# Performance work log

Hardware: AMD Instinct MI355X
Metric: run time of the kernel (lower is better)

Reference implementation:

```python
import jax, jax.numpy as jnp
import numpy as np

B, S, F, D, H, L = 32, 512, 10, 768, 12, 12
DK = D // H
FF = 4 * D
EPS = 1e-6
NEG = -1e9


def make_pe(window, d):
    pos = np.arange(window)[:, None].astype(np.float64)
    pe = np.zeros((window, d))
    ie = np.arange(0, d, 2)
    pe[:, 0::2] = np.sin(pos / 10000 ** (2 * ie / d))
    io = np.arange(1, d, 2)
    pe[:, 1::2] = np.cos(pos / 10000 ** (2 * (io + 1) / d))
    return jnp.asarray(pe, jnp.float32)


def setup_inputs() -> dict:
    key = jax.random.key(0)
    ks = jax.random.split(key, 20)
    s = 0.02
    inp = {
        "x": jax.random.normal(ks[0], (B, S, F), jnp.float32),
        "mask": jax.random.randint(ks[1], (B, S), 0, 2, jnp.int32),
        "w_emb": jax.random.normal(ks[2], (F, D), jnp.float32) * s,
        "b_emb": jnp.zeros((D,), jnp.float32),
        "pe": make_pe(S, D),
        "wq": jax.random.normal(ks[3], (L, D, D), jnp.float32) * s,
        "bq": jnp.zeros((L, D), jnp.float32),
        "wk": jax.random.normal(ks[4], (L, D, D), jnp.float32) * s,
        "bk": jnp.zeros((L, D), jnp.float32),
        "wv": jax.random.normal(ks[5], (L, D, D), jnp.float32) * s,
        "bv": jnp.zeros((L, D), jnp.float32),
        "wo": jax.random.normal(ks[6], (L, D, D), jnp.float32) * s,
        "bo": jnp.zeros((L, D), jnp.float32),
        "w1": jax.random.normal(ks[7], (L, D, FF), jnp.float32) * s,
        "b1": jnp.zeros((L, FF), jnp.float32),
        "w2": jax.random.normal(ks[8], (L, FF, D), jnp.float32) * s,
        "b2": jnp.zeros((L, D), jnp.float32),
        "ln1_a": jnp.ones((L, D), jnp.float32),
        "ln1_b": jnp.zeros((L, D), jnp.float32),
        "ln2_a": jnp.ones((L, D), jnp.float32),
        "ln2_b": jnp.zeros((L, D), jnp.float32),
    }
    return inp


def _ln(x, a, b):
    # torch-style: unbiased std (ddof=1) and divide by (std + eps)
    m = jnp.mean(x, -1, keepdims=True)
    var = jnp.sum((x - m) ** 2, -1, keepdims=True) / (x.shape[-1] - 1)
    return a * (x - m) / (jnp.sqrt(var) + EPS) + b


def _gelu(x):
    c = np.sqrt(2.0 / np.pi).astype(np.float32)
    return 0.5 * x * (1.0 + jnp.tanh(c * (x + 0.044715 * x ** 3)))


def _block(h, p, mask_b):
    wq, bq, wk, bk, wv, bv, wo, bo, w1, b1, w2, b2, a1, c1, a2, c2 = p
    y = _ln(h, a1, c1)
    q = (jnp.einsum('bsd,de->bse', y, wq) + bq).reshape(B, S, H, DK).transpose(0, 2, 1, 3)
    k = (jnp.einsum('bsd,de->bse', y, wk) + bk).reshape(B, S, H, DK).transpose(0, 2, 1, 3)
    v = (jnp.einsum('bsd,de->bse', y, wv) + bv).reshape(B, S, H, DK).transpose(0, 2, 1, 3)
    scores = jnp.einsum('bhqd,bhkd->bhqk', q, k) / np.sqrt(DK).astype(np.float32)
    scores = jnp.where(mask_b, scores, NEG)
    p_attn = jax.nn.softmax(scores, axis=-1)
    o = jnp.einsum('bhqk,bhkd->bhqd', p_attn, v).transpose(0, 2, 1, 3).reshape(B, S, D)
    h = h + (jnp.einsum('bsd,de->bse', o, wo) + bo)
    y2 = _ln(h, a2, c2)
    ff = jnp.einsum('bsf,fd->bsd', _gelu(jnp.einsum('bsd,df->bsf', y2, w1) + b1), w2) + b2
    return h + ff


def reference(x, mask, w_emb, b_emb, pe, wq, bq, wk, bk, wv, bv, wo, bo,
              w1, b1, w2, b2, ln1_a, ln1_b, ln2_a, ln2_b):
    # mask -> [B,1,1,S] boolean, broadcast over query positions (== repeat in torch)
    mask_b = (mask > 0)[:, None, None, :]
    h = jnp.einsum('bsf,fd->bsd', x, w_emb) + b_emb                 # InputEmbedding
    h = h * jnp.sqrt(jnp.float32(D)) + pe[None, :S]                 # PositionalEncoding
    params = (wq, bq, wk, bk, wv, bv, wo, bo, w1, b1, w2, b2,
              ln1_a, ln1_b, ln2_a, ln2_b)
    h, _ = jax.lax.scan(lambda c, p: (_block(c, p, mask_b), None), h, params)
    return h
```

## Files before the change

kernel.cpp:

```cpp
#include <hip/hip_runtime.h>
#include <cstdint>
#include <cstddef>

typedef unsigned short u16;
typedef __attribute__((ext_vector_type(8))) short s16x8;
typedef __attribute__((ext_vector_type(4))) float f32x4;

#define N_B 32
#define N_S 512
#define N_F 10
#define N_D 768
#define N_H 12
#define N_L 12
#define N_FF 3072
#define TOK (N_B*N_S)

__device__ __forceinline__ u16 f2bf(float f){
  union { float f; unsigned u; } x; x.f = f;
  unsigned r = x.u + 0x7fffu + ((x.u >> 16) & 1u);
  return (u16)(r >> 16);
}

__device__ __forceinline__ void gload16(const void* g, void* l){
  typedef const __attribute__((address_space(1))) unsigned GU;
  typedef __attribute__((address_space(3))) unsigned LU;
  __builtin_amdgcn_global_load_lds((GU*)(uintptr_t)g, (LU*)(uintptr_t)l, 16, 0, 0);
}

__global__ __launch_bounds__(256) void conv_t(const float* __restrict__ src,
                                              u16* __restrict__ dst, int K, int N)
{
  __shared__ float t[32][33];
  const size_t moff = (size_t)blockIdx.z * K * N;
  const float* s = src + moff;
  u16* d = dst + moff;
  const int k0 = blockIdx.x*32, n0 = blockIdx.y*32;
  const int tx = threadIdx.x, ty = threadIdx.y;
  #pragma unroll
  for (int i = 0; i < 32; i += 8)
    t[ty+i][tx] = s[(size_t)(k0+ty+i)*N + n0 + tx];
  __syncthreads();
  #pragma unroll
  for (int i = 0; i < 32; i += 8)
    d[(size_t)(n0+ty+i)*K + k0 + tx] = f2bf(t[tx][ty+i]);
}

__global__ __launch_bounds__(256) void embed_kernel(
    const float* __restrict__ x, const float* __restrict__ w,
    const float* __restrict__ bias, const float* __restrict__ pe,
    float* __restrict__ h)
{
  __shared__ float xr[N_F];
  const int row = blockIdx.x;
  const int s = row & (N_S-1);
  if (threadIdx.x < N_F) xr[threadIdx.x] = x[row*N_F + threadIdx.x];
  __syncthreads();
  for (int d = threadIdx.x; d < N_D; d += 256){
    float acc = bias[d];
    #pragma unroll
    for (int f = 0; f < N_F; f++) acc += xr[f]*w[f*N_D + d];
    h[(size_t)row*N_D + d] = acc*27.712812921102035f + pe[s*N_D + d];
  }
}

__global__ __launch_bounds__(256) void ln_kernel(
    const float* __restrict__ h, const float* __restrict__ ga,
    const float* __restrict__ gb, u16* __restrict__ y)
{
  const int lane = threadIdx.x & 63;
  const int row = blockIdx.x*4 + (threadIdx.x >> 6);
  const float* xr = h + (size_t)row*N_D;
  float v[12];
  float s = 0.f;
  #pragma unroll
  for (int i = 0; i < 12; i++){ v[i] = xr[lane + i*64]; s += v[i]; }
  #pragma unroll
  for (int o = 32; o > 0; o >>= 1) s += __shfl_xor(s, o, 64);
  const float m = s * (1.f/768.f);
  float q = 0.f;
  #pragma unroll
  for (int i = 0; i < 12; i++){ float d = v[i]-m; q += d*d; }
  #pragma unroll
  for (int o = 32; o > 0; o >>= 1) q += __shfl_xor(q, o, 64);
  const float inv = 1.f / (sqrtf(q*(1.f/767.f)) + 1e-6f);
  u16* yr = y + (size_t)row*N_D;
  #pragma unroll
  for (int i = 0; i < 12; i++){
    int c = lane + i*64;
    yr[c] = f2bf(ga[c]*(v[i]-m)*inv + gb[c]);
  }
}

template<int MODE>
__global__ __launch_bounds__(256) void gemm_bf16(
    const u16* __restrict__ A, const u16* __restrict__ Bt,
    const float* __restrict__ bias, void* __restrict__ outp,
    int M, int N, int K)
{
  __shared__ __align__(16) u16 As[128*32];
  __shared__ __align__(16) u16 Bs[128*32];
  const int tid = threadIdx.x;
  const int wid = tid >> 6, lane = tid & 63;
  const int bm = blockIdx.x, bn = blockIdx.y;
  const u16* Ag = A  + (size_t)bm*128*K;
  const u16* Bg = Bt + (size_t)bn*128*K;

  const int off0 = wid*2048 + lane*16;
  const int off1 = off0 + 1024;
  const int r0 = off0 >> 6, c0 = (off0 >> 4) & 3;
  const int r1 = off1 >> 6, c1 = (off1 >> 4) & 3;
  const u16* a0 = Ag + (size_t)r0*K + c0*8;
  const u16* a1 = Ag + (size_t)r1*K + c1*8;
  const u16* b0g = Bg + (size_t)r0*K + c0*8;
  const u16* b1g = Bg + (size_t)r1*K + c1*8;
  u16* lA0 = As + wid*1024;
  u16* lA1 = lA0 + 512;
  u16* lB0 = Bs + wid*1024;
  u16* lB1 = lB0 + 512;

  const int wm = (wid >> 1)*64, wn = (wid & 1)*64;
  const int rsel = lane & 15, kg = (lane >> 4)*8;

  f32x4 acc[4][4];
  const f32x4 z = {0.f, 0.f, 0.f, 0.f};
  #pragma unroll
  for (int i = 0; i < 4; i++)
    #pragma unroll
    for (int j = 0; j < 4; j++) acc[i][j] = z;

  for (int kt = 0; kt < K; kt += 32){
    __syncthreads();
    gload16(a0 + kt, lA0);
    gload16(a1 + kt, lA1);
    gload16(b0g + kt, lB0);
    gload16(b1g + kt, lB1);
    __syncthreads();
    s16x8 af[4], bfr[4];
    #pragma unroll
    for (int i = 0; i < 4; i++)
      af[i] = *(const s16x8*)(As + (wm + i*16 + rsel)*32 + kg);
    #pragma unroll
    for (int j = 0; j < 4; j++)
      bfr[j] = *(const s16x8*)(Bs + (wn + j*16 + rsel)*32 + kg);
    #pragma unroll
    for (int i = 0; i < 4; i++)
      #pragma unroll
      for (int j = 0; j < 4; j++)
        acc[i][j] = __builtin_amdgcn_mfma_f32_16x16x32_bf16(af[i], bfr[j], acc[i][j], 0, 0, 0);
  }

  const int m0 = bm*128 + wm;
  const int n0 = bn*128 + wn;
  #pragma unroll
  for (int i = 0; i < 4; i++){
    #pragma unroll
    for (int j = 0; j < 4; j++){
      const int colg = n0 + j*16 + rsel;
      const float bv = bias[colg];
      #pragma unroll
      for (int r = 0; r < 4; r++){
        const int rowg = m0 + i*16 + (lane >> 4)*4 + r;
        float val = acc[i][j][r] + bv;
        if (MODE == 0){
          const int bb = rowg >> 9, ss = rowg & 511, hh2 = colg >> 6, dk = colg & 63;
          ((u16*)outp)[(((size_t)(bb*N_H + hh2))*N_S + ss)*64 + dk] = f2bf(val);
        } else if (MODE == 2){
          const int bb = rowg >> 9, ss = rowg & 511, hh2 = colg >> 6, dk = colg & 63;
          ((u16*)outp)[(((size_t)(bb*N_H + hh2))*64 + dk)*N_S + ss] = f2bf(val);
        } else if (MODE == 3){
          ((float*)outp)[(size_t)rowg*N + colg] += val;
        } else if (MODE == 4){
          const float u = 0.7978845608028654f*(val + 0.044715f*val*val*val);
          const float e = __expf(2.f*u);
          const float th = 1.f - 2.f/(e + 1.f);
          ((u16*)outp)[(size_t)rowg*N + colg] = f2bf(0.5f*val*(1.f + th));
        }
      }
    }
  }
}

__global__ __launch_bounds__(256) void attn_kernel(
    const u16* __restrict__ q, const u16* __restrict__ k,
    const u16* __restrict__ vt, const int* __restrict__ mask,
    u16* __restrict__ o)
{
  __shared__ int mlds[N_S];
  __shared__ __align__(16) u16 plds[4*32*32];
  const int tid = threadIdx.x, wid = tid >> 6, lane = tid & 63;
  const int bh = blockIdx.x;
  const int b = bh / N_H, hh = bh % N_H;
  const int qt = blockIdx.y;
  mlds[tid]       = mask[b*N_S + tid];
  mlds[tid + 256] = mask[b*N_S + tid + 256];
  __syncthreads();

  const int q0 = qt*128 + wid*32;
  const u16* qb = q  + (size_t)bh*N_S*64;
  const u16* kb = k  + (size_t)bh*N_S*64;
  const u16* vb = vt + (size_t)bh*64*N_S;
  const int rsel = lane & 15, kg = (lane >> 4)*8;
  u16* pw = plds + wid*1024;

  s16x8 qa[2][2];
  #pragma unroll
  for (int i = 0; i < 2; i++)
    #pragma unroll
    for (int c = 0; c < 2; c++)
      qa[i][c] = *(const s16x8*)(qb + (size_t)(q0 + i*16 + rsel)*64 + c*32 + kg);

  f32x4 oc[2][4];
  const f32x4 z = {0.f,0.f,0.f,0.f};
  float mrun[2][4], lrun[2][4];
  #pragma unroll
  for (int i = 0; i < 2; i++){
    #pragma unroll
    for (int dj = 0; dj < 4; dj++) oc[i][dj] = z;
    #pragma unroll
    for (int r = 0; r < 4; r++){ mrun[i][r] = -3.0e38f; lrun[i][r] = 0.f; }
  }

  for (int kv = 0; kv < N_S; kv += 32){
    s16x8 kf[2][2];
    #pragma unroll
    for (int j = 0; j < 2; j++)
      #pragma unroll
      for (int c = 0; c < 2; c++)
        kf[j][c] = *(const s16x8*)(kb + (size_t)(kv + j*16 + rsel)*64 + c*32 + kg);
    f32x4 sc[2][2];
    #pragma unroll
    for (int i = 0; i < 2; i++)
      #pragma unroll
      for (int j = 0; j < 2; j++) sc[i][j] = z;
    #pragma unroll
    for (int i = 0; i < 2; i++)
      #pragma unroll
      for (int j = 0; j < 2; j++)
        #pragma unroll
        for (int c = 0; c < 2; c++)
          sc[i][j] = __builtin_amdgcn_mfma_f32_16x16x32_bf16(qa[i][c], kf[j][c], sc[i][j], 0, 0, 0);

    bool mok[2];
    mok[0] = mlds[kv + rsel] > 0;
    mok[1] = mlds[kv + 16 + rsel] > 0;
    #pragma unroll
    for (int i = 0; i < 2; i++)
      #pragma unroll
      for (int j = 0; j < 2; j++)
        #pragma unroll
        for (int r = 0; r < 4; r++)
          sc[i][j][r] = mok[j] ? sc[i][j][r]*0.125f : -1.0e9f;

    float tmx[2][4];
    #pragma unroll
    for (int i = 0; i < 2; i++)
      #pragma unroll
      for (int r = 0; r < 4; r++) tmx[i][r] = fmaxf(sc[i][0][r], sc[i][1][r]);
    #pragma unroll
    for (int off = 1; off < 16; off <<= 1)
      #pragma unroll
      for (int i = 0; i < 2; i++)
        #pragma unroll
        for (int r = 0; r < 4; r++)
          tmx[i][r] = fmaxf(tmx[i][r], __shfl_xor(tmx[i][r], off, 64));

    float alp[2][4], tsum[2][4];
    #pragma unroll
    for (int i = 0; i < 2; i++)
      #pragma unroll
      for (int r = 0; r < 4; r++){
        float nm = fmaxf(mrun[i][r], tmx[i][r]);
        alp[i][r] = __expf(mrun[i][r] - nm);
        mrun[i][r] = nm;
        float p0 = __expf(sc[i][0][r] - nm);
        float p1 = __expf(sc[i][1][r] - nm);
        sc[i][0][r] = p0; sc[i][1][r] = p1;
        tsum[i][r] = p0 + p1;
      }
    #pragma unroll
    for (int off = 1; off < 16; off <<= 1)
      #pragma unroll
      for (int i = 0; i < 2; i++)
        #pragma unroll
        for (int r = 0; r < 4; r++)
          tsum[i][r] += __shfl_xor(tsum[i][r], off, 64);
    #pragma unroll
    for (int i = 0; i < 2; i++)
      #pragma unroll
      for (int r = 0; r < 4; r++)
        lrun[i][r] = lrun[i][r]*alp[i][r] + tsum[i][r];
    #pragma unroll
    for (int i = 0; i < 2; i++)
      #pragma unroll
      for (int dj = 0; dj < 4; dj++)
        #pragma unroll
        for (int r = 0; r < 4; r++)
          oc[i][dj][r] *= alp[i][r];

    #pragma unroll
    for (int i = 0; i < 2; i++)
      #pragma unroll
      for (int j = 0; j < 2; j++)
        #pragma unroll
        for (int r = 0; r < 4; r++)
          pw[(i*16 + (lane >> 4)*4 + r)*32 + j*16 + rsel] = f2bf(sc[i][j][r]);
    s16x8 pa[2];
    #pragma unroll
    for (int i = 0; i < 2; i++)
      pa[i] = *(const s16x8*)(pw + (i*16 + rsel)*32 + kg);
    s16x8 vf[4];
    #pragma unroll
    for (int dj = 0; dj < 4; dj++)
      vf[dj] = *(const s16x8*)(vb + (size_t)(dj*16 + rsel)*N_S + kv + kg);
    #pragma unroll
    for (int i = 0; i < 2; i++)
      #pragma unroll
      for (int dj = 0; dj < 4; dj++)
        oc[i][dj] = __builtin_amdgcn_mfma_f32_16x16x32_bf16(pa[i], vf[dj], oc[i][dj], 0, 0, 0);
  }

  #pragma unroll
  for (int i = 0; i < 2; i++){
    float rinv[4];
    #pragma unroll
    for (int r = 0; r < 4; r++) rinv[r] = 1.f / lrun[i][r];
    #pragma unroll
    for (int dj = 0; dj < 4; dj++)
      #pragma unroll
      for (int r = 0; r < 4; r++){
        const int srow = q0 + i*16 + (lane >> 4)*4 + r;
        const int col = hh*64 + dj*16 + rsel;
        o[((size_t)b*N_S + srow)*N_D + col] = f2bf(oc[i][dj][r]*rinv[r]);
      }
  }
}

extern "C" void kernel_launch(void* const* d_in, const int* in_sizes, int n_in,
                              void* d_out, int out_size, void* d_ws, size_t ws_size,
                              hipStream_t stream)
{
  const float* x     = (const float*)d_in[0];
  const int*   mask  = (const int*)  d_in[1];
  const float* w_emb = (const float*)d_in[2];
  const float* b_emb = (const float*)d_in[3];
  const float* pe    = (const float*)d_in[4];
  const float* wq    = (const float*)d_in[5];
  const float* bq    = (const float*)d_in[6];
  const float* wk    = (const float*)d_in[7];
  const float* bk    = (const float*)d_in[8];
  const float* wv    = (const float*)d_in[9];
  const float* bv    = (const float*)d_in[10];
  const float* wo    = (const float*)d_in[11];
  const float* bo    = (const float*)d_in[12];
  const float* w1    = (const float*)d_in[13];
  const float* b1    = (const float*)d_in[14];
  const float* w2    = (const float*)d_in[15];
  const float* b2    = (const float*)d_in[16];
  const float* ln1a  = (const float*)d_in[17];
  const float* ln1b  = (const float*)d_in[18];
  const float* ln2a  = (const float*)d_in[19];
  const float* ln2b  = (const float*)d_in[20];

  char* ws = (char*)d_ws;
  const size_t WMAT = (size_t)N_D*N_D;
  const size_t WFF  = (size_t)N_D*N_FF;
  u16* wq_t = (u16*)ws;
  u16* wk_t = wq_t + (size_t)N_L*WMAT;
  u16* wv_t = wk_t + (size_t)N_L*WMAT;
  u16* wo_t = wv_t + (size_t)N_L*WMAT;
  u16* w1_t = wo_t + (size_t)N_L*WMAT;
  u16* w2_t = w1_t + (size_t)N_L*WFF;
  u16* act  = w2_t + (size_t)N_L*WFF;
  u16* big  = act  + (size_t)TOK*N_D;
  u16* qb   = big;
  u16* kb   = qb  + (size_t)TOK*N_D;
  u16* vtb  = kb  + (size_t)TOK*N_D;
  u16* gbuf = big;
  float* hbuf = (float*)d_out;

  dim3 tb(32, 8);
  conv_t<<<dim3(24,24,12), tb, 0, stream>>>(wq, wq_t, N_D, N_D);
  conv_t<<<dim3(24,24,12), tb, 0, stream>>>(wk, wk_t, N_D, N_D);
  conv_t<<<dim3(24,24,12), tb, 0, stream>>>(wv, wv_t, N_D, N_D);
  conv_t<<<dim3(24,24,12), tb, 0, stream>>>(wo, wo_t, N_D, N_D);
  conv_t<<<dim3(24,96,12), tb, 0, stream>>>(w1, w1_t, N_D, N_FF);
  conv_t<<<dim3(96,24,12), tb, 0, stream>>>(w2, w2_t, N_FF, N_D);

  embed_kernel<<<TOK, 256, 0, stream>>>(x, w_emb, b_emb, pe, hbuf);

  const dim3 g768(TOK/128, N_D/128);
  const dim3 g3072(TOK/128, N_FF/128);
  for (int l = 0; l < N_L; l++){
    ln_kernel<<<TOK/4, 256, 0, stream>>>(hbuf, ln1a + l*N_D, ln1b + l*N_D, act);
    gemm_bf16<0><<<g768, 256, 0, stream>>>(act, wq_t + l*WMAT, bq + l*N_D, qb,  TOK, N_D, N_D);
    gemm_bf16<0><<<g768, 256, 0, stream>>>(act, wk_t + l*WMAT, bk + l*N_D, kb,  TOK, N_D, N_D);
    gemm_bf16<2><<<g768, 256, 0, stream>>>(act, wv_t + l*WMAT, bv + l*N_D, vtb, TOK, N_D, N_D);
    attn_kernel<<<dim3(N_B*N_H, 4), 256, 0, stream>>>(qb, kb, vtb, mask, act);
    gemm_bf16<3><<<g768, 256, 0, stream>>>(act, wo_t + l*WMAT, bo + l*N_D, hbuf, TOK, N_D, N_D);
    ln_kernel<<<TOK/4, 256, 0, stream>>>(hbuf, ln2a + l*N_D, ln2b + l*N_D, act);
    gemm_bf16<4><<<g3072, 256, 0, stream>>>(act, w1_t + l*WFF, b1 + l*N_FF, gbuf, TOK, N_FF, N_D);
    gemm_bf16<3><<<g768, 256, 0, stream>>>(gbuf, w2_t + l*WFF, b2 + l*N_D, hbuf, TOK, N_D, N_FF);
  }
}
```

Before: 7.353 ms.

## Triple-buffer GEMM LDS loads with swizzled layout and raise MFMA priority in attention

The bf16 GEMM now uses a three-stage LDS ring, with global-to-LDS loads issued three K-tiles ahead. Explicit vmcnt waits and barriers replace the two syncthreads per K step, so load latency is meant to overlap with MFMA work. A XOR swizzle on the 16-byte column chunk is added to reduce LDS bank conflicts on fragment reads, and launch bounds request 3 blocks per CU. In the attention kernel, the MFMA sections are wrapped in s_setprio to favour matrix issue. The costs are more LDS per block (48KB), hand-written wait counts that must match the load count, and register pressure under the new occupancy hint.

```diff
diff --git a/kernel.cpp b/kernel.cpp
--- a/kernel.cpp
+++ b/kernel.cpp
@@ -27,6 +27,14 @@
   __builtin_amdgcn_global_load_lds((GU*)(uintptr_t)g, (LU*)(uintptr_t)l, 16, 0, 0);
 }
 
+#define VMW8  asm volatile("s_waitcnt vmcnt(8)" ::: "memory")
+#define VMW4  asm volatile("s_waitcnt vmcnt(4)" ::: "memory")
+#define VMW0  asm volatile("s_waitcnt vmcnt(0)" ::: "memory")
+#define LGKM0 asm volatile("s_waitcnt lgkmcnt(0)" ::: "memory")
+#define CFENCE asm volatile("" ::: "memory")
+#define BARF  do { __builtin_amdgcn_s_barrier(); CFENCE; } while(0)
+#define SCHED0 __builtin_amdgcn_sched_barrier(0)
+
 __global__ __launch_bounds__(256) void conv_t(const float* __restrict__ src,
                                               u16* __restrict__ dst, int K, int N)
 {
@@ -92,13 +100,12 @@
 }
 
 template<int MODE>
-__global__ __launch_bounds__(256) void gemm_bf16(
+__global__ __launch_bounds__(256, 3) void gemm_bf16(
     const u16* __restrict__ A, const u16* __restrict__ Bt,
     const float* __restrict__ bias, void* __restrict__ outp,
     int M, int N, int K)
 {
-  __shared__ __align__(16) u16 As[128*32];
-  __shared__ __align__(16) u16 Bs[128*32];
+  __shared__ __align__(16) u16 lds[3*8192];
   const int tid = threadIdx.x;
   const int wid = tid >> 6, lane = tid & 63;
   const int bm = blockIdx.x, bn = blockIdx.y;
@@ -109,18 +116,27 @@
   const int off1 = off0 + 1024;
   const int r0 = off0 >> 6, c0 = (off0 >> 4) & 3;
   const int r1 = off1 >> 6, c1 = (off1 >> 4) & 3;
-  const u16* a0 = Ag + (size_t)r0*K + c0*8;
-  const u16* a1 = Ag + (size_t)r1*K + c1*8;
-  const u16* b0g = Bg + (size_t)r0*K + c0*8;
-  const u16* b1g = Bg + (size_t)r1*K + c1*8;
-  u16* lA0 = As + wid*1024;
-  u16* lA1 = lA0 + 512;
-  u16* lB0 = Bs + wid*1024;
-  u16* lB1 = lB0 + 512;
+  const int c0s = c0 ^ ((r0 >> 1) & 3);
+  const int c1s = c1 ^ ((r1 >> 1) & 3);
+  const u16* a0 = Ag + (size_t)r0*K + c0s*8;
+  const u16* a1 = Ag + (size_t)r1*K + c1s*8;
+  const u16* b0 = Bg + (size_t)r0*K + c0s*8;
+  const u16* b1 = Bg + (size_t)r1*K + c1s*8;
+  const int ldst0 = wid*1024;
+  const int ldst1 = ldst0 + 512;
 
   const int wm = (wid >> 1)*64, wn = (wid & 1)*64;
   const int rsel = lane & 15, kg = (lane >> 4)*8;
 
+  int aoff[4], boff[4];
+  #pragma unroll
+  for (int i = 0; i < 4; i++){
+    const int ra = wm + i*16 + rsel;
+    aoff[i] = ra*32 + (kg ^ (((ra >> 1) & 3) << 3));
+    const int rb = wn + i*16 + rsel;
+    boff[i] = 4096 + rb*32 + (kg ^ (((rb >> 1) & 3) << 3));
+  }
+
   f32x4 acc[4][4];
   const f32x4 z = {0.f, 0.f, 0.f, 0.f};
   #pragma unroll
@@ -128,26 +144,57 @@
     #pragma unroll
     for (int j = 0; j < 4; j++) acc[i][j] = z;
 
-  for (int kt = 0; kt < K; kt += 32){
-    __syncthreads();
-    gload16(a0 + kt, lA0);
-    gload16(a1 + kt, lA1);
-    gload16(b0g + kt, lB0);
-    gload16(b1g + kt, lB1);
-    __syncthreads();
-    s16x8 af[4], bfr[4];
-    #pragma unroll
-    for (int i = 0; i < 4; i++)
-      af[i] = *(const s16x8*)(As + (wm + i*16 + rsel)*32 + kg);
-    #pragma unroll
-    for (int j = 0; j < 4; j++)
-      bfr[j] = *(const s16x8*)(Bs + (wn + j*16 + rsel)*32 + kg);
-    #pragma unroll
-    for (int i = 0; i < 4; i++)
-      #pragma unroll
-      for (int j = 0; j < 4; j++)
+#define STAGE(S, KT) do { u16* Lp = lds + (S)*8192;       \
+    gload16(a0 + (KT), Lp + ldst0);                       \
+    gload16(a1 + (KT), Lp + ldst1);                       \
+    gload16(b0 + (KT), Lp + 4096 + ldst0);                \
+    gload16(b1 + (KT), Lp + 4096 + ldst1); } while(0)
+
+#define FRAGS(S)                                          \
+    const u16* Lp = lds + (S)*8192;                       \
+    s16x8 af[4], bfr[4];                                  \
+    _Pragma("unroll")                                     \
+    for (int i = 0; i < 4; i++) af[i]  = *(const s16x8*)(Lp + aoff[i]); \
+    _Pragma("unroll")                                     \
+    for (int j = 0; j < 4; j++) bfr[j] = *(const s16x8*)(Lp + boff[j]);
+
+#define MFMA16                                            \
+    _Pragma("unroll")                                     \
+    for (int i = 0; i < 4; i++)                           \
+      _Pragma("unroll")                                   \
+      for (int j = 0; j < 4; j++)                         \
         acc[i][j] = __builtin_amdgcn_mfma_f32_16x16x32_bf16(af[i], bfr[j], acc[i][j], 0, 0, 0);
-  }
+
+  const int nt = K >> 5;
+  STAGE(0, 0); STAGE(1, 32); STAGE(2, 64);
+  int sl = 0;
+  int t = 0;
+  for (; t + 3 < nt; ++t){
+    VMW8; BARF;
+    {
+      FRAGS(sl);
+      LGKM0;
+      BARF;
+      SCHED0;
+      STAGE(sl, (t+3)*32);
+      SCHED0;
+      MFMA16;
+    }
+    sl = (sl == 2) ? 0 : sl + 1;
+  }
+  {
+    VMW8; BARF;
+    { FRAGS(sl); LGKM0; MFMA16; }
+    sl = (sl == 2) ? 0 : sl + 1;
+    VMW4; BARF;
+    { FRAGS(sl); LGKM0; MFMA16; }
+    sl = (sl == 2) ? 0 : sl + 1;
+    VMW0; BARF;
+    { FRAGS(sl); LGKM0; MFMA16; }
+  }
+#undef STAGE
+#undef FRAGS
+#undef MFMA16
 
   const int m0 = bm*128 + wm;
   const int n0 = bn*128 + wn;
@@ -232,6 +279,7 @@
     for (int i = 0; i < 2; i++)
       #pragma unroll
       for (int j = 0; j < 2; j++) sc[i][j] = z;
+    __builtin_amdgcn_s_setprio(1);
     #pragma unroll
     for (int i = 0; i < 2; i++)
       #pragma unroll
@@ -239,6 +287,7 @@
         #pragma unroll
         for (int c = 0; c < 2; c++)
           sc[i][j] = __builtin_amdgcn_mfma_f32_16x16x32_bf16(qa[i][c], kf[j][c], sc[i][j], 0, 0, 0);
+    __builtin_amdgcn_s_setprio(0);
 
     bool mok[2];
     mok[0] = mlds[kv + rsel] > 0;
@@ -312,11 +361,13 @@
     #pragma unroll
     for (int dj = 0; dj < 4; dj++)
       vf[dj] = *(const s16x8*)(vb + (size_t)(dj*16 + rsel)*N_S + kv + kg);
+    __builtin_amdgcn_s_setprio(1);
     #pragma unroll
     for (int i = 0; i < 2; i++)
       #pragma unroll
       for (int dj = 0; dj < 4; dj++)
         oc[i][dj] = __builtin_amdgcn_mfma_f32_16x16x32_bf16(pa[i], vf[dj], oc[i][dj], 0, 0, 0);
+    __builtin_amdgcn_s_setprio(0);
   }
 
   #pragma unroll
```

Result: faster. 6.207 ms (-15.6%).
